# Kernel optimization log

Hardware: AMD Instinct MI355X
Metric: run time of the kernel (lower is better)

## Reference

```python
import jax, jax.numpy as jnp
import numpy as np

N, E, H, HEADS, T = 40000, 320000, 128, 4, 3
DH = H // HEADS


def setup_inputs() -> dict:
    key = jax.random.key(0)
    ks = jax.random.split(key, 32)
    f32 = jnp.float32

    def w(k, shape, s=0.05):
        return (s * jax.random.normal(k, shape)).astype(f32)

    inp = {
        "x": jax.random.normal(ks[0], (N, H), dtype=f32),
        "edge_index": jax.random.randint(ks[1], (2, E), 0, N, dtype=jnp.int32),
        "edge_attr": 0.1 * jax.random.normal(ks[2], (E, H), dtype=f32),
        "wq": w(ks[3], (H, H)), "bq": w(ks[4], (H,)),
        "wk": w(ks[5], (H, H)), "bk": w(ks[6], (H,)),
        "wv": w(ks[7], (H, H)), "bv": w(ks[8], (H,)),
        "w_ao": w(ks[9], (H, H)), "b_ao": w(ks[10], (H,)),
        "ln1_g": jnp.ones((H,), f32), "ln1_b": jnp.zeros((H,), f32),
        "w_int": w(ks[11], (4 * H, H)), "b_int": w(ks[12], (4 * H,)),
        "w_out": w(ks[13], (H, 4 * H)), "b_out": w(ks[14], (H,)),
        "ln2_g": jnp.ones((H,), f32), "ln2_b": jnp.zeros((H,), f32),
        "w_ih": w(ks[15], (3 * H, H)), "w_hh": w(ks[16], (3 * H, H)),
        "b_ih": w(ks[17], (3 * H,)), "b_hh": w(ks[18], (3 * H,)),
        "ln3_g": jnp.ones((H,), f32), "ln3_b": jnp.zeros((H,), f32),
    }
    return inp


def _ln(x, g, b, eps=1e-12):
    u = jnp.mean(x, axis=-1, keepdims=True)
    s = jnp.mean((x - u) ** 2, axis=-1, keepdims=True)
    return g * (x - u) / jnp.sqrt(s + eps) + b


def _gat(x, src, dst, edge_attr, wq, bq, wk, bk, wv, bv):
    # per-edge gather: x_i = target features, x_j = source features (+ pseudo)
    x_i = x[dst]                       # [E, H]
    x_j = x[src] + edge_attr           # [E, H]
    q = (x_i @ wq.T + bq).reshape(-1, HEADS, DH)
    k = (x_j @ wk.T + bk).reshape(-1, HEADS, DH)
    v = (x_j @ wv.T + bv).reshape(-1, HEADS, DH)
    alpha = jnp.sum(q * k, axis=-1) / jnp.sqrt(jnp.float32(DH))  # [E, HEADS]
    # segment softmax over incoming edges of each target node
    m = jax.ops.segment_max(alpha, dst, num_segments=N)
    m = jnp.where(jnp.isfinite(m), m, jnp.zeros_like(m))
    a = jnp.exp(alpha - m[dst])
    s = jax.ops.segment_sum(a, dst, num_segments=N)
    a = a / (s[dst] + 1e-16)
    out = jax.ops.segment_sum(a[..., None] * v, dst, num_segments=N)  # [N, HEADS, DH]
    return out.reshape(N, H)


def reference(x, edge_index, edge_attr, wq, bq, wk, bk, wv, bv,
              w_ao, b_ao, ln1_g, ln1_b, w_int, b_int, w_out, b_out,
              ln2_g, ln2_b, w_ih, w_hh, b_ih, b_hh, ln3_g, ln3_b):
    src, dst = edge_index[0], edge_index[1]
    h = x  # GRU hidden state, [N, H] (seq_len=1, batch=N)
    for _ in range(T):
        att = _gat(x, src, dst, edge_attr, wq, bq, wk, bk, wv, bv)
        att = _ln(att @ w_ao.T + b_ao + x, ln1_g, ln1_b)
        inter = jax.nn.gelu(att @ w_int.T + b_int, approximate=False)
        m = _ln(inter @ w_out.T + b_out + att, ln2_g, ln2_b)
        # single-step GRU (torch gate order: r, z, n)
        gi = m @ w_ih.T + b_ih
        gh = h @ w_hh.T + b_hh
        ir, iz, inn = jnp.split(gi, 3, axis=-1)
        hr, hz, hn = jnp.split(gh, 3, axis=-1)
        r = jax.nn.sigmoid(ir + hr)
        z = jax.nn.sigmoid(iz + hz)
        n = jnp.tanh(inn + r * hn)
        h = (1.0 - z) * n + z * h
        x = _ln(h, ln3_g, ln3_b)
    return x
```

## Files before the change

### kernel.cpp

```cpp
#include <hip/hip_runtime.h>
#include <hip/hip_bf16.h>
#include <math.h>

#define N_NODES 40000
#define N_EDGES 320000
#define T_ITERS 3

typedef __attribute__((ext_vector_type(8))) short short8;
typedef __attribute__((ext_vector_type(4))) short short4v;
typedef __attribute__((ext_vector_type(4))) float f32x4;

static __device__ __forceinline__ short f2bf(float f) {
    union { float f; unsigned u; } x; x.f = f;
    unsigned r = (x.u + 0x7fffu + ((x.u >> 16) & 1u)) >> 16;
    return (short)r;
}
static __device__ __forceinline__ float bf2f(short s) {
    union { unsigned u; float f; } x; x.u = ((unsigned)(unsigned short)s) << 16;
    return x.f;
}

__global__ __launch_bounds__(256) void qkv_kernel(
    const short* __restrict__ A, const short* __restrict__ W,
    const float* __restrict__ bias, short* __restrict__ Cb)
{
    __shared__ __align__(16) short smem[64 * 136];
    short* As = smem;
    short* Ws = smem + 64 * 40;
    short* Cs = smem;

    const int tid  = threadIdx.x;
    const int lane = tid & 63, wid = tid >> 6;
    const int wm = wid & 1, wn = wid >> 1;
    const int t16 = lane & 15, quad = lane >> 4;
    const long blockM = (long)blockIdx.x * 64;
    const int colBase = blockIdx.y * 128;

    f32x4 acc[2][4];
    for (int i = 0; i < 2; i++)
        for (int j = 0; j < 4; j++)
            acc[i][j] = (f32x4){0.f, 0.f, 0.f, 0.f};

    for (int k0 = 0; k0 < 128; k0 += 32) {
        {
            const int r = tid >> 2, c = (tid & 3) * 8;
            *(short8*)&As[r * 40 + c] = *(const short8*)(A + (blockM + r) * 128 + k0 + c);
        }
        for (int gg = 0; gg < 2; gg++) {
            const int chunk = tid + gg * 256;
            const int r = chunk >> 2, c = (chunk & 3) * 8;
            *(short8*)&Ws[r * 40 + c] =
                *(const short8*)(W + (long)(colBase + r) * 128 + k0 + c);
        }
        __syncthreads();
        short8 a0 = *(const short8*)&As[(wm * 32 + t16) * 40 + quad * 8];
        short8 a1 = *(const short8*)&As[(wm * 32 + 16 + t16) * 40 + quad * 8];
        for (int ni = 0; ni < 4; ni++) {
            short8 bf = *(const short8*)&Ws[(wn * 64 + ni * 16 + t16) * 40 + quad * 8];
            acc[0][ni] = __builtin_amdgcn_mfma_f32_16x16x32_bf16(a0, bf, acc[0][ni], 0, 0, 0);
            acc[1][ni] = __builtin_amdgcn_mfma_f32_16x16x32_bf16(a1, bf, acc[1][ni], 0, 0, 0);
        }
        __syncthreads();
    }

    for (int mi = 0; mi < 2; mi++)
        for (int ni = 0; ni < 4; ni++) {
            const int col = wn * 64 + ni * 16 + t16;
            const float bb = bias[colBase + col];
            for (int r = 0; r < 4; r++) {
                const int row = wm * 32 + mi * 16 + quad * 4 + r;
                Cs[row * 136 + col] = f2bf(acc[mi][ni][r] + bb);
            }
        }
    __syncthreads();
    for (int it = 0; it < 4; it++) {
        const int idx = it * 256 + tid;
        const int row = idx >> 4, c8 = idx & 15;
        *(short8*)(Cb + (blockM + row) * 384 + colBase + c8 * 8) =
            *(const short8*)&Cs[row * 136 + c8 * 8];
    }
}

__global__ __launch_bounds__(256, 4) void ekv_kernel(
    const float* __restrict__ ea, const short* __restrict__ Wkv,
    const float* __restrict__ bkv, const int* __restrict__ eids,
    short* __restrict__ EKV)
{
    __shared__ __align__(16) char smem[64 * 136 * 2 + 256 * 40 * 2];
    short* As = (short*)smem;
    short* Ws = (short*)(smem + 64 * 136 * 2);
    short* Cs = (short*)smem;

    const int tid  = threadIdx.x;
    const int lane = tid & 63, wid = tid >> 6;
    const int t16 = lane & 15, quad = lane >> 4;
    const long blockM = (long)blockIdx.x * 64;

    {
        const int r = tid >> 2, c0 = (tid & 3) * 32;
        const long e = eids[blockM + r];
        const float* gp = ea + e * 128 + c0;
        for (int half = 0; half < 2; half++) {
            float4 v0 = *(const float4*)(gp + half * 16);
            float4 v1 = *(const float4*)(gp + half * 16 + 4);
            float4 v2 = *(const float4*)(gp + half * 16 + 8);
            float4 v3 = *(const float4*)(gp + half * 16 + 12);
            short8 s0, s1;
            s0[0] = f2bf(v0.x); s0[1] = f2bf(v0.y); s0[2] = f2bf(v0.z); s0[3] = f2bf(v0.w);
            s0[4] = f2bf(v1.x); s0[5] = f2bf(v1.y); s0[6] = f2bf(v1.z); s0[7] = f2bf(v1.w);
            s1[0] = f2bf(v2.x); s1[1] = f2bf(v2.y); s1[2] = f2bf(v2.z); s1[3] = f2bf(v2.w);
            s1[4] = f2bf(v3.x); s1[5] = f2bf(v3.y); s1[6] = f2bf(v3.z); s1[7] = f2bf(v3.w);
            *(short8*)&As[r * 136 + c0 + half * 16]     = s0;
            *(short8*)&As[r * 136 + c0 + half * 16 + 8] = s1;
        }
    }

    f32x4 acc[4][4];
    for (int i = 0; i < 4; i++)
        for (int j = 0; j < 4; j++)
            acc[i][j] = (f32x4){0.f, 0.f, 0.f, 0.f};

    for (int k0 = 0; k0 < 128; k0 += 32) {
        for (int g = 0; g < 4; g++) {
            const int idx = tid + g * 256;
            const int r = idx >> 2, c = (idx & 3) * 8;
            *(short8*)&Ws[r * 40 + c] = *(const short8*)(Wkv + (long)r * 128 + k0 + c);
        }
        __syncthreads();
        short8 a[4];
        for (int mi = 0; mi < 4; mi++)
            a[mi] = *(const short8*)&As[(mi * 16 + t16) * 136 + k0 + quad * 8];
        for (int ni = 0; ni < 4; ni++) {
            short8 bf = *(const short8*)&Ws[(wid * 64 + ni * 16 + t16) * 40 + quad * 8];
            for (int mi = 0; mi < 4; mi++)
                acc[mi][ni] = __builtin_amdgcn_mfma_f32_16x16x32_bf16(a[mi], bf, acc[mi][ni], 0, 0, 0);
        }
        __syncthreads();
    }

    for (int mi = 0; mi < 4; mi++)
        for (int ni = 0; ni < 4; ni++) {
            const int col = wid * 64 + ni * 16 + t16;
            const float bv_ = bkv[col];
            for (int r = 0; r < 4; r++) {
                const int row = mi * 16 + quad * 4 + r;
                Cs[row * 276 + col] = f2bf(acc[mi][ni][r] + bv_);
            }
        }
    __syncthreads();
    for (int it = 0; it < 8; it++) {
        const int idx = it * 256 + tid;
        const int row = idx >> 5, c8 = idx & 31;
        *(short8*)(EKV + (blockM + row) * 256 + c8 * 8) = *(const short8*)&Cs[row * 276 + c8 * 8];
    }
}

__global__ __launch_bounds__(256) void edge_attn_kernel(
    const short* __restrict__ QKVb, const short* __restrict__ EKV,
    const int* __restrict__ rowptr, const int* __restrict__ esrc,
    short* __restrict__ outb)
{
    const int wid = threadIdx.x >> 6, lane = threadIdx.x & 63;
    const int n = blockIdx.x * 4 + wid;
    if (n >= N_NODES) return;
    const int g = lane >> 3, l8 = lane & 7;
    const int d0 = l8 * 16;
    const float scale = 0.17677669529663687f;

    short8 q0 = *(const short8*)&QKVb[(long)n * 384 + d0];
    short8 q1 = *(const short8*)&QKVb[(long)n * 384 + d0 + 8];
    float qf[16];
#pragma unroll
    for (int j = 0; j < 8; j++) { qf[j] = bf2f(q0[j]); qf[8 + j] = bf2f(q1[j]); }

    const int beg = rowptr[n], end = rowptr[n + 1];
    float acc[16];
#pragma unroll
    for (int j = 0; j < 16; j++) acc[j] = 0.f;
    float ssum = 0.f;

    for (int i0 = beg; i0 < end; i0 += 8) {
        const int i = i0 + g;
        const bool valid = i < end;
        const long ii = valid ? i : beg;
        const long s = esrc[ii];
        short8 k0 = *(const short8*)&EKV[ii * 256 + d0];
        short8 k1 = *(const short8*)&EKV[ii * 256 + d0 + 8];
        short8 xk0 = *(const short8*)&QKVb[s * 384 + 128 + d0];
        short8 xk1 = *(const short8*)&QKVb[s * 384 + 128 + d0 + 8];
        short8 v0 = *(const short8*)&EKV[ii * 256 + 128 + d0];
        short8 v1 = *(const short8*)&EKV[ii * 256 + 128 + d0 + 8];
        short8 xv0 = *(const short8*)&QKVb[s * 384 + 256 + d0];
        short8 xv1 = *(const short8*)&QKVb[s * 384 + 256 + d0 + 8];
        float dot = 0.f;
#pragma unroll
        for (int j = 0; j < 8; j++) {
            dot += qf[j] * (bf2f(k0[j]) + bf2f(xk0[j]));
            dot += qf[8 + j] * (bf2f(k1[j]) + bf2f(xk1[j]));
        }
        dot += __shfl_xor(dot, 1);
        float a = valid ? __expf(dot * scale) : 0.f;
        ssum += a;
#pragma unroll
        for (int j = 0; j < 8; j++) {
            acc[j]     += a * (bf2f(v0[j]) + bf2f(xv0[j]));
            acc[8 + j] += a * (bf2f(v1[j]) + bf2f(xv1[j]));
        }
    }
#pragma unroll
    for (int o = 8; o < 64; o <<= 1) {
#pragma unroll
        for (int j = 0; j < 16; j++) acc[j] += __shfl_xor(acc[j], o);
        ssum += __shfl_xor(ssum, o);
    }
    if (g == 0) {
        float inv = 1.0f / (ssum + 1e-16f);
        short8 o0, o1;
#pragma unroll
        for (int j = 0; j < 8; j++) { o0[j] = f2bf(acc[j] * inv); o1[j] = f2bf(acc[8 + j] * inv); }
        *(short8*)&outb[(long)n * 128 + d0] = o0;
        *(short8*)&outb[(long)n * 128 + d0 + 8] = o1;
    }
}

__global__ __launch_bounds__(256) void ffn_kernel(
    const short* __restrict__ attraw, const short* __restrict__ x,
    const short* __restrict__ Wao, const short* __restrict__ Wint,
    const short* __restrict__ Wout, const float* __restrict__ b_ao,
    const float* __restrict__ b_int, const float* __restrict__ b_out,
    const float* __restrict__ ln1_g, const float* __restrict__ ln1_b,
    const float* __restrict__ ln2_g, const float* __restrict__ ln2_b,
    short* __restrict__ Mout)
{
    __shared__ __align__(16) short As[64 * 136];
    __shared__ __align__(16) short Is[64 * 136];
    __shared__ __align__(16) short Ws[128 * 40];

    const int tid  = threadIdx.x;
    const int lane = tid & 63, wid = tid >> 6;
    const int t16 = lane & 15, quad = lane >> 4;
    const long blockM = (long)blockIdx.x * 64;

    {
        const int r = tid >> 2, c = (tid & 3) * 32;
        const long gr = blockM + r;
        for (int j = 0; j < 4; j++) {
            *(short8*)&As[r * 136 + c + j * 8] = *(const short8*)(x + gr * 128 + c + j * 8);
            *(short8*)&Is[r * 136 + c + j * 8] = *(const short8*)(attraw + gr * 128 + c + j * 8);
        }
    }
    __syncthreads();

    f32x4 acc0[8];
    for (int j = 0; j < 8; j++) acc0[j] = (f32x4){0.f, 0.f, 0.f, 0.f};
    for (int k0 = 0; k0 < 128; k0 += 32) {
        const int r = tid >> 1, c = (tid & 1) * 16;
        *(short8*)&Ws[r * 40 + c]     = *(const short8*)(Wao + (long)r * 128 + k0 + c);
        *(short8*)&Ws[r * 40 + c + 8] = *(const short8*)(Wao + (long)r * 128 + k0 + c + 8);
        __syncthreads();
        short8 a = *(const short8*)&Is[(wid * 16 + t16) * 136 + k0 + quad * 8];
        for (int ni = 0; ni < 8; ni++) {
            short8 bf = *(const short8*)&Ws[(ni * 16 + t16) * 40 + quad * 8];
            acc0[ni] = __builtin_amdgcn_mfma_f32_16x16x32_bf16(a, bf, acc0[ni], 0, 0, 0);
        }
        __syncthreads();
    }
    for (int r = 0; r < 4; r++) {
        const int row = wid * 16 + quad * 4 + r;
        float vals[8];
        float s = 0.f;
        for (int ni = 0; ni < 8; ni++) {
            const int col = ni * 16 + t16;
            float v = acc0[ni][r] + b_ao[col] + bf2f(As[row * 136 + col]);
            vals[ni] = v;
            s += v;
        }
        for (int o = 1; o < 16; o <<= 1) s += __shfl_xor(s, o);
        float u = s * (1.0f / 128.0f);
        float vs = 0.f;
        for (int ni = 0; ni < 8; ni++) { float d = vals[ni] - u; vals[ni] = d; vs += d * d; }
        for (int o = 1; o < 16; o <<= 1) vs += __shfl_xor(vs, o);
        float rstd = rsqrtf(vs * (1.0f / 128.0f) + 1e-12f);
        for (int ni = 0; ni < 8; ni++) {
            const int col = ni * 16 + t16;
            As[row * 136 + col] = f2bf(ln1_g[col] * vals[ni] * rstd + ln1_b[col]);
        }
    }
    __syncthreads();

    f32x4 acc2[8];
    for (int j = 0; j < 8; j++) acc2[j] = (f32x4){0.f, 0.f, 0.f, 0.f};
    for (int kc = 0; kc < 4; kc++) {
        f32x4 acc1[8];
        for (int j = 0; j < 8; j++) acc1[j] = (f32x4){0.f, 0.f, 0.f, 0.f};
        for (int k0 = 0; k0 < 128; k0 += 32) {
            const int r = tid >> 1, c = (tid & 1) * 16;
            *(short8*)&Ws[r * 40 + c] =
                *(const short8*)(Wint + (long)(kc * 128 + r) * 128 + k0 + c);
            *(short8*)&Ws[r * 40 + c + 8] =
                *(const short8*)(Wint + (long)(kc * 128 + r) * 128 + k0 + c + 8);
            __syncthreads();
            short8 a = *(const short8*)&As[(wid * 16 + t16) * 136 + k0 + quad * 8];
            for (int ni = 0; ni < 8; ni++) {
                short8 bf = *(const short8*)&Ws[(ni * 16 + t16) * 40 + quad * 8];
                acc1[ni] = __builtin_amdgcn_mfma_f32_16x16x32_bf16(a, bf, acc1[ni], 0, 0, 0);
            }
            __syncthreads();
        }
        for (int ni = 0; ni < 8; ni++) {
            const int col = ni * 16 + t16;
            const float bi = b_int[kc * 128 + col];
            for (int r = 0; r < 4; r++) {
                const int row = wid * 16 + quad * 4 + r;
                float v = acc1[ni][r] + bi;
                v = 0.5f * v * (1.0f + erff(v * 0.70710678118654752f));
                Is[row * 136 + col] = f2bf(v);
            }
        }
        __syncthreads();
        for (int k0 = 0; k0 < 128; k0 += 32) {
            const int r = tid >> 1, c = (tid & 1) * 16;
            *(short8*)&Ws[r * 40 + c] =
                *(const short8*)(Wout + (long)r * 512 + kc * 128 + k0 + c);
            *(short8*)&Ws[r * 40 + c + 8] =
                *(const short8*)(Wout + (long)r * 512 + kc * 128 + k0 + c + 8);
            __syncthreads();
            short8 a = *(const short8*)&Is[(wid * 16 + t16) * 136 + k0 + quad * 8];
            for (int ni = 0; ni < 8; ni++) {
                short8 bf = *(const short8*)&Ws[(ni * 16 + t16) * 40 + quad * 8];
                acc2[ni] = __builtin_amdgcn_mfma_f32_16x16x32_bf16(a, bf, acc2[ni], 0, 0, 0);
            }
            __syncthreads();
        }
    }

    for (int r = 0; r < 4; r++) {
        const int row = wid * 16 + quad * 4 + r;
        const long gr = blockM + row;
        float vals[8];
        float s = 0.f;
        for (int ni = 0; ni < 8; ni++) {
            const int col = ni * 16 + t16;
            float v = acc2[ni][r] + b_out[col] + bf2f(As[row * 136 + col]);
            vals[ni] = v;
            s += v;
        }
        for (int o = 1; o < 16; o <<= 1) s += __shfl_xor(s, o);
        float u = s * (1.0f / 128.0f);
        float vs = 0.f;
        for (int ni = 0; ni < 8; ni++) { float d = vals[ni] - u; vals[ni] = d; vs += d * d; }
        for (int o = 1; o < 16; o <<= 1) vs += __shfl_xor(vs, o);
        float rstd = rsqrtf(vs * (1.0f / 128.0f) + 1e-12f);
        for (int ni = 0; ni < 8; ni++) {
            const int col = ni * 16 + t16;
            Mout[gr * 128 + col] = f2bf(ln2_g[col] * vals[ni] * rstd + ln2_b[col]);
        }
    }
}

template<bool FINAL>
__global__ __launch_bounds__(256) void gru_kernel(
    const short* __restrict__ m, const short* __restrict__ h,
    const short* __restrict__ Wg, const float* __restrict__ bg,
    const float* __restrict__ g3, const float* __restrict__ b3,
    short* __restrict__ hout, void* __restrict__ xout)
{
    __shared__ __align__(16) char smem[64 * 520 * 2];
    short* As = (short*)smem;
    short* Ws = (short*)(smem + 64 * 40 * 2);
    short* Os = (short*)smem;

    const int tid  = threadIdx.x;
    const int lane = tid & 63, wid = tid >> 6;
    const int t16 = lane & 15, quad = lane >> 4;
    const long blockM = (long)blockIdx.x * 64;

    f32x4 acc[4][8];
    for (int i = 0; i < 4; i++)
        for (int j = 0; j < 8; j++)
            acc[i][j] = (f32x4){0.f, 0.f, 0.f, 0.f};

    for (int k0 = 0; k0 < 256; k0 += 32) {
        const short* src = (k0 < 128) ? m : h;
        {
            const int r = tid >> 2, c = (tid & 3) * 8;
            *(short8*)&As[r * 40 + c] =
                *(const short8*)(src + (blockM + r) * 128 + (k0 & 127) + c);
        }
        for (int g = 0; g < 8; g++) {
            const int idx = tid + g * 256;
            const int r = idx >> 2, c = (idx & 3) * 8;
            *(short8*)&Ws[r * 40 + c] = *(const short8*)(Wg + (long)r * 256 + k0 + c);
        }
        __syncthreads();
        short8 a[4];
        for (int mi = 0; mi < 4; mi++)
            a[mi] = *(const short8*)&As[(mi * 16 + t16) * 40 + quad * 8];
        for (int ni = 0; ni < 8; ni++) {
            short8 bf = *(const short8*)&Ws[(wid * 128 + ni * 16 + t16) * 40 + quad * 8];
            for (int mi = 0; mi < 4; mi++)
                acc[mi][ni] = __builtin_amdgcn_mfma_f32_16x16x32_bf16(a[mi], bf, acc[mi][ni], 0, 0, 0);
        }
        __syncthreads();
    }

    for (int mi = 0; mi < 4; mi++)
        for (int ni = 0; ni < 8; ni++) {
            const int col = wid * 128 + ni * 16 + t16;
            const float bb = bg[col];
            for (int r = 0; r < 4; r++) {
                const int row = mi * 16 + quad * 4 + r;
                Os[row * 520 + col] = f2bf(acc[mi][ni][r] + bb);
            }
        }
    __syncthreads();

    {
        const int row = tid >> 2;
        const int c0 = (tid & 3) * 32;
        const long gr = blockM + row;
        float hv[32];
        for (int j = 0; j < 4; j++) {
            short8 hpv = *(const short8*)(h + gr * 128 + c0 + j * 8);
            short8 orv = *(const short8*)&Os[row * 520 + c0 + j * 8];
            short8 ozv = *(const short8*)&Os[row * 520 + 128 + c0 + j * 8];
            short8 onv = *(const short8*)&Os[row * 520 + 256 + c0 + j * 8];
            short8 ohv = *(const short8*)&Os[row * 520 + 384 + c0 + j * 8];
            for (int q = 0; q < 8; q++) {
                float rr = 1.f / (1.f + __expf(-bf2f(orv[q])));
                float zz = 1.f / (1.f + __expf(-bf2f(ozv[q])));
                float nn = tanhf(bf2f(onv[q]) + rr * bf2f(ohv[q]));
                float hpq = bf2f(hpv[q]);
                hv[j * 8 + q] = (1.f - zz) * nn + zz * hpq;
            }
        }
        float s = 0.f;
        for (int j = 0; j < 32; j++) s += hv[j];
        s += __shfl_xor(s, 1); s += __shfl_xor(s, 2);
        float u = s * (1.0f / 128.0f);
        float vs = 0.f;
        for (int j = 0; j < 32; j++) { float d = hv[j] - u; vs += d * d; }
        vs += __shfl_xor(vs, 1); vs += __shfl_xor(vs, 2);
        float rstd = rsqrtf(vs * (1.0f / 128.0f) + 1e-12f);
        for (int j = 0; j < 4; j++) {
            short8 o;
            for (int q = 0; q < 8; q++) o[q] = f2bf(hv[j * 8 + q]);
            *(short8*)(hout + gr * 128 + c0 + j * 8) = o;
        }
        if (FINAL) {
            float* xo = (float*)xout;
            for (int j = 0; j < 8; j++) {
                float4 o;
                o.x = g3[c0 + j * 4 + 0] * (hv[j * 4 + 0] - u) * rstd + b3[c0 + j * 4 + 0];
                o.y = g3[c0 + j * 4 + 1] * (hv[j * 4 + 1] - u) * rstd + b3[c0 + j * 4 + 1];
                o.z = g3[c0 + j * 4 + 2] * (hv[j * 4 + 2] - u) * rstd + b3[c0 + j * 4 + 2];
                o.w = g3[c0 + j * 4 + 3] * (hv[j * 4 + 3] - u) * rstd + b3[c0 + j * 4 + 3];
                *(float4*)&xo[gr * 128 + c0 + j * 4] = o;
            }
        } else {
            short* xo = (short*)xout;
            for (int j = 0; j < 4; j++) {
                short8 o;
                for (int q = 0; q < 8; q++) {
                    const int c = c0 + j * 8 + q;
                    o[q] = f2bf(g3[c] * (hv[j * 8 + q] - u) * rstd + b3[c]);
                }
                *(short8*)(xo + gr * 128 + c0 + j * 8) = o;
            }
        }
    }
}

__global__ void count_kernel(const int* __restrict__ dst, int* __restrict__ cnt) {
    int e = blockIdx.x * 256 + threadIdx.x;
    if (e < N_EDGES) atomicAdd(&cnt[dst[e]], 1);
}

__global__ __launch_bounds__(1024) void scan_kernel(const int* __restrict__ cnt,
                                                    int* __restrict__ rowptr) {
    __shared__ int lds[1024];
    const int tid = threadIdx.x;
    const int CH = 40;
    const int base = tid * CH;
    int sum = 0;
    for (int j = 0; j < CH; j++) { int i = base + j; if (i < N_NODES) sum += cnt[i]; }
    lds[tid] = sum;
    __syncthreads();
    for (int off = 1; off < 1024; off <<= 1) {
        int v = (tid >= off) ? lds[tid - off] : 0;
        __syncthreads();
        lds[tid] += v;
        __syncthreads();
    }
    int run = lds[tid] - sum;
    for (int j = 0; j < CH; j++) {
        int i = base + j;
        if (i < N_NODES) { rowptr[i] = run; run += cnt[i]; }
    }
    if (tid == 1023) rowptr[N_NODES] = lds[1023];
}

__global__ void fill_kernel(const int* __restrict__ src, const int* __restrict__ dst,
                            const int* __restrict__ rowptr, int* __restrict__ wo,
                            int* __restrict__ esrc, int* __restrict__ eids) {
    int e = blockIdx.x * 256 + threadIdx.x;
    if (e < N_EDGES) {
        int d = dst[e];
        int pos = atomicAdd(&wo[d], 1);
        int slot = rowptr[d] + pos;
        esrc[slot] = src[e];
        eids[slot] = e;
    }
}

__global__ void sortfix_kernel(const int* __restrict__ rowptr,
                               int* __restrict__ eids, int* __restrict__ esrc) {
    int n = blockIdx.x * 256 + threadIdx.x;
    if (n >= N_NODES) return;
    const int beg = rowptr[n], end = rowptr[n + 1];
    for (int i = beg + 1; i < end; i++) {
        int ke = eids[i], ks = esrc[i];
        int j = i - 1;
        while (j >= beg && eids[j] > ke) {
            eids[j + 1] = eids[j];
            esrc[j + 1] = esrc[j];
            j--;
        }
        eids[j + 1] = ke;
        esrc[j + 1] = ks;
    }
}

__global__ void cvt_kernel(const float* __restrict__ s, short* __restrict__ d, int n) {
    int i = (blockIdx.x * 256 + threadIdx.x) * 4;
    if (i < n) {
        float4 v = *(const float4*)(s + i);
        short4v sv;
        sv.x = f2bf(v.x); sv.y = f2bf(v.y); sv.z = f2bf(v.z); sv.w = f2bf(v.w);
        *(short4v*)(d + i) = sv;
    }
}
__global__ void bias_cat_kernel(const float* __restrict__ bq, const float* __restrict__ bk,
                                const float* __restrict__ bv, float* __restrict__ bqkv,
                                float* __restrict__ bkv) {
    int i = blockIdx.x * 256 + threadIdx.x;
    if (i < 384) bqkv[i] = (i < 128) ? bq[i] : 0.0f;
    if (i < 256) bkv[i] = (i < 128) ? bk[i] : bv[i - 128];
}
__global__ void build_wg_kernel(const float* __restrict__ wih, const float* __restrict__ whh,
                                const float* __restrict__ bih, const float* __restrict__ bhh,
                                short* __restrict__ Wg, float* __restrict__ bg) {
    int idx = blockIdx.x * 256 + threadIdx.x;
    if (idx < 512 * 256) {
        int r = idx >> 8, k = idx & 255;
        float v;
        if (r < 256)      v = (k < 128) ? wih[r * 128 + k] : whh[r * 128 + k - 128];
        else if (r < 384) v = (k < 128) ? wih[r * 128 + k] : 0.f;
        else              v = (k < 128) ? 0.f : whh[(r - 128) * 128 + k - 128];
        Wg[idx] = f2bf(v);
    }
    if (idx < 512) {
        float b;
        if (idx < 256)      b = bih[idx] + bhh[idx];
        else if (idx < 384) b = bih[idx];
        else                b = bhh[idx - 128];
        bg[idx] = b;
    }
}

extern "C" void kernel_launch(void* const* d_in, const int* in_sizes, int n_in,
                              void* d_out, int out_size, void* d_ws, size_t ws_size,
                              hipStream_t stream) {
    const float* x_in  = (const float*)d_in[0];
    const int*   eidx  = (const int*)d_in[1];
    const float* ea    = (const float*)d_in[2];
    const float* wq    = (const float*)d_in[3];
    const float* bq    = (const float*)d_in[4];
    const float* wk    = (const float*)d_in[5];
    const float* bk    = (const float*)d_in[6];
    const float* wv    = (const float*)d_in[7];
    const float* bv    = (const float*)d_in[8];
    const float* w_ao  = (const float*)d_in[9];
    const float* b_ao  = (const float*)d_in[10];
    const float* ln1_g = (const float*)d_in[11];
    const float* ln1_b = (const float*)d_in[12];
    const float* w_int = (const float*)d_in[13];
    const float* b_int = (const float*)d_in[14];
    const float* w_out = (const float*)d_in[15];
    const float* b_out = (const float*)d_in[16];
    const float* ln2_g = (const float*)d_in[17];
    const float* ln2_b = (const float*)d_in[18];
    const float* w_ih  = (const float*)d_in[19];
    const float* w_hh  = (const float*)d_in[20];
    const float* b_ih  = (const float*)d_in[21];
    const float* b_hh  = (const float*)d_in[22];
    const float* ln3_g = (const float*)d_in[23];
    const float* ln3_b = (const float*)d_in[24];
    const int* srcv = eidx;
    const int* dstv = eidx + N_EDGES;

    char* ws = (char*)d_ws;
    size_t off = 0;
    auto alloc = [&](size_t bytes) -> void* {
        void* p = ws + off;
        off += (bytes + 255) & ~(size_t)255;
        return p;
    };
    short* EKV  = (short*)alloc((size_t)N_EDGES * 256 * 2);
    short* Wcat = (short*)alloc(384 * 128 * 2);
    short* Wao  = (short*)alloc(128 * 128 * 2);
    short* Wint = (short*)alloc(512 * 128 * 2);
    short* Wout = (short*)alloc(128 * 512 * 2);
    short* Wg   = (short*)alloc(512 * 256 * 2);
    float* bqkv = (float*)alloc(384 * 4);
    float* bkv  = (float*)alloc(256 * 4);
    float* bg   = (float*)alloc(512 * 4);
    int* cnt    = (int*)alloc((size_t)N_NODES * 4);
    int* wo     = (int*)alloc((size_t)N_NODES * 4);
    int* rowptr = (int*)alloc((size_t)(N_NODES + 1) * 4);
    int* esrc   = (int*)alloc((size_t)N_EDGES * 4);
    int* eids   = (int*)alloc((size_t)N_EDGES * 4);
    short* xb     = (short*)alloc((size_t)N_NODES * 128 * 2);
    short* QKVb   = (short*)alloc((size_t)N_NODES * 384 * 2);
    short* attraw = (short*)alloc((size_t)N_NODES * 128 * 2);
    short* mbuf   = (short*)alloc((size_t)N_NODES * 128 * 2);
    short* hbuf   = (short*)alloc((size_t)N_NODES * 128 * 2);
    short* xbuf   = (short*)alloc((size_t)N_NODES * 128 * 2);
    if (off > ws_size) return;

    cvt_kernel<<<16, 256, 0, stream>>>(wq, Wcat, 16384);
    cvt_kernel<<<16, 256, 0, stream>>>(wk, Wcat + 16384, 16384);
    cvt_kernel<<<16, 256, 0, stream>>>(wv, Wcat + 32768, 16384);
    cvt_kernel<<<16, 256, 0, stream>>>(w_ao, Wao, 16384);
    cvt_kernel<<<64, 256, 0, stream>>>(w_int, Wint, 65536);
    cvt_kernel<<<64, 256, 0, stream>>>(w_out, Wout, 65536);
    cvt_kernel<<<5000, 256, 0, stream>>>(x_in, xb, N_NODES * 128);
    bias_cat_kernel<<<2, 256, 0, stream>>>(bq, bk, bv, bqkv, bkv);
    build_wg_kernel<<<512, 256, 0, stream>>>(w_ih, w_hh, b_ih, b_hh, Wg, bg);

    hipMemsetAsync(cnt, 0, (size_t)N_NODES * 4, stream);
    hipMemsetAsync(wo, 0, (size_t)N_NODES * 4, stream);
    count_kernel<<<1250, 256, 0, stream>>>(dstv, cnt);
    scan_kernel<<<1, 1024, 0, stream>>>(cnt, rowptr);
    fill_kernel<<<1250, 256, 0, stream>>>(srcv, dstv, rowptr, wo, esrc, eids);
    sortfix_kernel<<<157, 256, 0, stream>>>(rowptr, eids, esrc);

    ekv_kernel<<<5000, 256, 0, stream>>>(ea, Wcat + 128 * 128, bkv, eids, EKV);

    const short* xcur = xb;
    const short* hcur = xb;
    for (int t = 0; t < T_ITERS; t++) {
        qkv_kernel<<<dim3(625, 3), 256, 0, stream>>>(xcur, Wcat, bqkv, QKVb);
        edge_attn_kernel<<<10000, 256, 0, stream>>>(QKVb, EKV, rowptr, esrc, attraw);
        ffn_kernel<<<625, 256, 0, stream>>>(
            attraw, xcur, Wao, Wint, Wout, b_ao, b_int, b_out,
            ln1_g, ln1_b, ln2_g, ln2_b, mbuf);
        if (t == T_ITERS - 1)
            gru_kernel<true><<<625, 256, 0, stream>>>(
                mbuf, hcur, Wg, bg, ln3_g, ln3_b, hbuf, d_out);
        else
            gru_kernel<false><<<625, 256, 0, stream>>>(
                mbuf, hcur, Wg, bg, ln3_g, ln3_b, hbuf, xbuf);
        xcur = xbuf;
        hcur = hbuf;
    }
}
```

Before: 1.191 ms.

## Keep hidden state and x in fp32 and restructure GRU kernel without LDS

Hidden state and the normalized x now stay in fp32 instead of bf16, with the qkv and GRU kernels converting to bf16 on load. The qkv kernel stages the whole 64x128 A tile in shared memory once rather than per k-chunk. The GRU kernel is rewritten so each wave keeps its A fragments in registers and reads weights straight from global memory, with the gates and layernorm computed in registers without the LDS round trip. The goal appears to be accuracy plus lower LDS and sync overhead, at the cost of twice the bytes for x and h traffic and uncached per-wave weight reads.

```diff
diff --git a/kernel.cpp b/kernel.cpp
--- a/kernel.cpp
+++ b/kernel.cpp
@@ -21,12 +21,12 @@
 }
 
 __global__ __launch_bounds__(256) void qkv_kernel(
-    const short* __restrict__ A, const short* __restrict__ W,
+    const float* __restrict__ A, const short* __restrict__ W,
     const float* __restrict__ bias, short* __restrict__ Cb)
 {
-    __shared__ __align__(16) short smem[64 * 136];
+    __shared__ __align__(16) short smem[64 * 136 + 128 * 40];
     short* As = smem;
-    short* Ws = smem + 64 * 40;
+    short* Ws = smem + 64 * 136;
     short* Cs = smem;
 
     const int tid  = threadIdx.x;
@@ -36,16 +36,30 @@
     const long blockM = (long)blockIdx.x * 64;
     const int colBase = blockIdx.y * 128;
 
+    {
+        const int r = tid >> 2, c0 = (tid & 3) * 32;
+        const float* gp = A + (blockM + r) * 128 + c0;
+        for (int half = 0; half < 2; half++) {
+            float4 v0 = *(const float4*)(gp + half * 16);
+            float4 v1 = *(const float4*)(gp + half * 16 + 4);
+            float4 v2 = *(const float4*)(gp + half * 16 + 8);
+            float4 v3 = *(const float4*)(gp + half * 16 + 12);
+            short8 s0, s1;
+            s0[0] = f2bf(v0.x); s0[1] = f2bf(v0.y); s0[2] = f2bf(v0.z); s0[3] = f2bf(v0.w);
+            s0[4] = f2bf(v1.x); s0[5] = f2bf(v1.y); s0[6] = f2bf(v1.z); s0[7] = f2bf(v1.w);
+            s1[0] = f2bf(v2.x); s1[1] = f2bf(v2.y); s1[2] = f2bf(v2.z); s1[3] = f2bf(v2.w);
+            s1[4] = f2bf(v3.x); s1[5] = f2bf(v3.y); s1[6] = f2bf(v3.z); s1[7] = f2bf(v3.w);
+            *(short8*)&As[r * 136 + c0 + half * 16]     = s0;
+            *(short8*)&As[r * 136 + c0 + half * 16 + 8] = s1;
+        }
+    }
+
     f32x4 acc[2][4];
     for (int i = 0; i < 2; i++)
         for (int j = 0; j < 4; j++)
             acc[i][j] = (f32x4){0.f, 0.f, 0.f, 0.f};
 
     for (int k0 = 0; k0 < 128; k0 += 32) {
-        {
-            const int r = tid >> 2, c = (tid & 3) * 8;
-            *(short8*)&As[r * 40 + c] = *(const short8*)(A + (blockM + r) * 128 + k0 + c);
-        }
         for (int gg = 0; gg < 2; gg++) {
             const int chunk = tid + gg * 256;
             const int r = chunk >> 2, c = (chunk & 3) * 8;
@@ -53,8 +67,8 @@
                 *(const short8*)(W + (long)(colBase + r) * 128 + k0 + c);
         }
         __syncthreads();
-        short8 a0 = *(const short8*)&As[(wm * 32 + t16) * 40 + quad * 8];
-        short8 a1 = *(const short8*)&As[(wm * 32 + 16 + t16) * 40 + quad * 8];
+        short8 a0 = *(const short8*)&As[(wm * 32 + t16) * 136 + k0 + quad * 8];
+        short8 a1 = *(const short8*)&As[(wm * 32 + 16 + t16) * 136 + k0 + quad * 8];
         for (int ni = 0; ni < 4; ni++) {
             short8 bf = *(const short8*)&Ws[(wn * 64 + ni * 16 + t16) * 40 + quad * 8];
             acc[0][ni] = __builtin_amdgcn_mfma_f32_16x16x32_bf16(a0, bf, acc[0][ni], 0, 0, 0);
@@ -224,7 +238,7 @@
 }
 
 __global__ __launch_bounds__(256) void ffn_kernel(
-    const short* __restrict__ attraw, const short* __restrict__ x,
+    const short* __restrict__ attraw, const float* __restrict__ x,
     const short* __restrict__ Wao, const short* __restrict__ Wint,
     const short* __restrict__ Wout, const float* __restrict__ b_ao,
     const float* __restrict__ b_int, const float* __restrict__ b_out,
@@ -244,10 +258,8 @@
     {
         const int r = tid >> 2, c = (tid & 3) * 32;
         const long gr = blockM + r;
-        for (int j = 0; j < 4; j++) {
-            *(short8*)&As[r * 136 + c + j * 8] = *(const short8*)(x + gr * 128 + c + j * 8);
+        for (int j = 0; j < 4; j++)
             *(short8*)&Is[r * 136 + c + j * 8] = *(const short8*)(attraw + gr * 128 + c + j * 8);
-        }
     }
     __syncthreads();
 
@@ -265,13 +277,15 @@
         }
         __syncthreads();
     }
+    float attv[4][8];
     for (int r = 0; r < 4; r++) {
         const int row = wid * 16 + quad * 4 + r;
+        const long gr = blockM + row;
         float vals[8];
         float s = 0.f;
         for (int ni = 0; ni < 8; ni++) {
             const int col = ni * 16 + t16;
-            float v = acc0[ni][r] + b_ao[col] + bf2f(As[row * 136 + col]);
+            float v = acc0[ni][r] + b_ao[col] + x[gr * 128 + col];
             vals[ni] = v;
             s += v;
         }
@@ -283,7 +297,9 @@
         float rstd = rsqrtf(vs * (1.0f / 128.0f) + 1e-12f);
         for (int ni = 0; ni < 8; ni++) {
             const int col = ni * 16 + t16;
-            As[row * 136 + col] = f2bf(ln1_g[col] * vals[ni] * rstd + ln1_b[col]);
+            float av = ln1_g[col] * vals[ni] * rstd + ln1_b[col];
+            attv[r][ni] = av;
+            As[row * 136 + col] = f2bf(av);
         }
     }
     __syncthreads();
@@ -341,7 +357,7 @@
         float s = 0.f;
         for (int ni = 0; ni < 8; ni++) {
             const int col = ni * 16 + t16;
-            float v = acc2[ni][r] + b_out[col] + bf2f(As[row * 136 + col]);
+            float v = acc2[ni][r] + b_out[col] + attv[r][ni];
             vals[ni] = v;
             s += v;
         }
@@ -358,115 +374,106 @@
     }
 }
 
-template<bool FINAL>
-__global__ __launch_bounds__(256) void gru_kernel(
-    const short* __restrict__ m, const short* __restrict__ h,
+__global__ __launch_bounds__(256, 2) void gru_kernel(
+    const short* __restrict__ m, const float* __restrict__ h,
     const short* __restrict__ Wg, const float* __restrict__ bg,
     const float* __restrict__ g3, const float* __restrict__ b3,
-    short* __restrict__ hout, void* __restrict__ xout)
+    float* __restrict__ hout, float* __restrict__ xout)
 {
-    __shared__ __align__(16) char smem[64 * 520 * 2];
-    short* As = (short*)smem;
-    short* Ws = (short*)(smem + 64 * 40 * 2);
-    short* Os = (short*)smem;
-
     const int tid  = threadIdx.x;
     const int lane = tid & 63, wid = tid >> 6;
     const int t16 = lane & 15, quad = lane >> 4;
     const long blockM = (long)blockIdx.x * 64;
+    const long rowA = blockM + wid * 16 + t16;
+
+    short8 a[8];
+#pragma unroll
+    for (int k0 = 0; k0 < 4; k0++)
+        a[k0] = *(const short8*)(m + rowA * 128 + k0 * 32 + quad * 8);
+#pragma unroll
+    for (int k0 = 4; k0 < 8; k0++) {
+        const float* hp8 = h + rowA * 128 + (k0 - 4) * 32 + quad * 8;
+        float4 f0 = *(const float4*)(hp8);
+        float4 f1 = *(const float4*)(hp8 + 4);
+        short8 s;
+        s[0] = f2bf(f0.x); s[1] = f2bf(f0.y); s[2] = f2bf(f0.z); s[3] = f2bf(f0.w);
+        s[4] = f2bf(f1.x); s[5] = f2bf(f1.y); s[6] = f2bf(f1.z); s[7] = f2bf(f1.w);
+        a[k0] = s;
+    }
 
     f32x4 acc[4][8];
-    for (int i = 0; i < 4; i++)
-        for (int j = 0; j < 8; j++)
-            acc[i][j] = (f32x4){0.f, 0.f, 0.f, 0.f};
-
-    for (int k0 = 0; k0 < 256; k0 += 32) {
-        const short* src = (k0 < 128) ? m : h;
-        {
-            const int r = tid >> 2, c = (tid & 3) * 8;
-            *(short8*)&As[r * 40 + c] =
-                *(const short8*)(src + (blockM + r) * 128 + (k0 & 127) + c);
-        }
-        for (int g = 0; g < 8; g++) {
-            const int idx = tid + g * 256;
-            const int r = idx >> 2, c = (idx & 3) * 8;
-            *(short8*)&Ws[r * 40 + c] = *(const short8*)(Wg + (long)r * 256 + k0 + c);
-        }
-        __syncthreads();
-        short8 a[4];
-        for (int mi = 0; mi < 4; mi++)
-            a[mi] = *(const short8*)&As[(mi * 16 + t16) * 40 + quad * 8];
-        for (int ni = 0; ni < 8; ni++) {
-            short8 bf = *(const short8*)&Ws[(wid * 128 + ni * 16 + t16) * 40 + quad * 8];
-            for (int mi = 0; mi < 4; mi++)
-                acc[mi][ni] = __builtin_amdgcn_mfma_f32_16x16x32_bf16(a[mi], bf, acc[mi][ni], 0, 0, 0);
-        }
-        __syncthreads();
-    }
-
-    for (int mi = 0; mi < 4; mi++)
-        for (int ni = 0; ni < 8; ni++) {
-            const int col = wid * 128 + ni * 16 + t16;
-            const float bb = bg[col];
-            for (int r = 0; r < 4; r++) {
-                const int row = mi * 16 + quad * 4 + r;
-                Os[row * 520 + col] = f2bf(acc[mi][ni][r] + bb);
+#pragma unroll
+    for (int g = 0; g < 4; g++)
+#pragma unroll
+        for (int c16 = 0; c16 < 8; c16++)
+            acc[g][c16] = (f32x4){0.f, 0.f, 0.f, 0.f};
+
+#pragma unroll
+    for (int g = 0; g < 4; g++)
+#pragma unroll
+        for (int c16 = 0; c16 < 8; c16++) {
+            const short* wr = Wg + (long)(g * 128 + c16 * 16 + t16) * 256 + quad * 8;
+#pragma unroll
+            for (int k0 = 0; k0 < 8; k0++) {
+                short8 w = *(const short8*)(wr + k0 * 32);
+                acc[g][c16] = __builtin_amdgcn_mfma_f32_16x16x32_bf16(a[k0], w, acc[g][c16], 0, 0, 0);
             }
         }
-    __syncthreads();
-
-    {
-        const int row = tid >> 2;
-        const int c0 = (tid & 3) * 32;
-        const long gr = blockM + row;
-        float hv[32];
-        for (int j = 0; j < 4; j++) {
-            short8 hpv = *(const short8*)(h + gr * 128 + c0 + j * 8);
-            short8 orv = *(const short8*)&Os[row * 520 + c0 + j * 8];
-            short8 ozv = *(const short8*)&Os[row * 520 + 128 + c0 + j * 8];
-            short8 onv = *(const short8*)&Os[row * 520 + 256 + c0 + j * 8];
-            short8 ohv = *(const short8*)&Os[row * 520 + 384 + c0 + j * 8];
-            for (int q = 0; q < 8; q++) {
-                float rr = 1.f / (1.f + __expf(-bf2f(orv[q])));
-                float zz = 1.f / (1.f + __expf(-bf2f(ozv[q])));
-                float nn = tanhf(bf2f(onv[q]) + rr * bf2f(ohv[q]));
-                float hpq = bf2f(hpv[q]);
-                hv[j * 8 + q] = (1.f - zz) * nn + zz * hpq;
-            }
-        }
-        float s = 0.f;
-        for (int j = 0; j < 32; j++) s += hv[j];
-        s += __shfl_xor(s, 1); s += __shfl_xor(s, 2);
-        float u = s * (1.0f / 128.0f);
-        float vs = 0.f;
-        for (int j = 0; j < 32; j++) { float d = hv[j] - u; vs += d * d; }
-        vs += __shfl_xor(vs, 1); vs += __shfl_xor(vs, 2);
-        float rstd = rsqrtf(vs * (1.0f / 128.0f) + 1e-12f);
-        for (int j = 0; j < 4; j++) {
-            short8 o;
-            for (int q = 0; q < 8; q++) o[q] = f2bf(hv[j * 8 + q]);
-            *(short8*)(hout + gr * 128 + c0 + j * 8) = o;
-        }
-        if (FINAL) {
-            float* xo = (float*)xout;
-            for (int j = 0; j < 8; j++) {
-                float4 o;
-                o.x = g3[c0 + j * 4 + 0] * (hv[j * 4 + 0] - u) * rstd + b3[c0 + j * 4 + 0];
-                o.y = g3[c0 + j * 4 + 1] * (hv[j * 4 + 1] - u) * rstd + b3[c0 + j * 4 + 1];
-                o.z = g3[c0 + j * 4 + 2] * (hv[j * 4 + 2] - u) * rstd + b3[c0 + j * 4 + 2];
-                o.w = g3[c0 + j * 4 + 3] * (hv[j * 4 + 3] - u) * rstd + b3[c0 + j * 4 + 3];
-                *(float4*)&xo[gr * 128 + c0 + j * 4] = o;
-            }
-        } else {
-            short* xo = (short*)xout;
-            for (int j = 0; j < 4; j++) {
-                short8 o;
-                for (int q = 0; q < 8; q++) {
-                    const int c = c0 + j * 8 + q;
-                    o[q] = f2bf(g3[c] * (hv[j * 8 + q] - u) * rstd + b3[c]);
-                }
-                *(short8*)(xo + gr * 128 + c0 + j * 8) = o;
-            }
+
+    const long rowBase = blockM + wid * 16 + quad * 4;
+    float hv[8][4];
+    float sums[4] = {0.f, 0.f, 0.f, 0.f};
+#pragma unroll
+    for (int c16 = 0; c16 < 8; c16++) {
+        const int col = c16 * 16 + t16;
+        const float b_r = bg[col];
+        const float b_z = bg[col + 128];
+        const float b_i = bg[col + 256];
+        const float b_h = bg[col + 384];
+#pragma unroll
+        for (int r = 0; r < 4; r++) {
+            float rr = 1.f / (1.f + __expf(-(acc[0][c16][r] + b_r)));
+            float zz = 1.f / (1.f + __expf(-(acc[1][c16][r] + b_z)));
+            float nn = tanhf(acc[2][c16][r] + b_i + rr * (acc[3][c16][r] + b_h));
+            float hp = h[(rowBase + r) * 128 + col];
+            float v = (1.f - zz) * nn + zz * hp;
+            hv[c16][r] = v;
+            sums[r] += v;
+        }
+    }
+#pragma unroll
+    for (int r = 0; r < 4; r++)
+#pragma unroll
+        for (int o = 1; o < 16; o <<= 1) sums[r] += __shfl_xor(sums[r], o);
+    float u[4], vsum[4] = {0.f, 0.f, 0.f, 0.f};
+#pragma unroll
+    for (int r = 0; r < 4; r++) u[r] = sums[r] * (1.0f / 128.0f);
+#pragma unroll
+    for (int c16 = 0; c16 < 8; c16++)
+#pragma unroll
+        for (int r = 0; r < 4; r++) {
+            float d = hv[c16][r] - u[r];
+            vsum[r] += d * d;
+        }
+#pragma unroll
+    for (int r = 0; r < 4; r++) {
+#pragma unroll
+        for (int o = 1; o < 16; o <<= 1) vsum[r] += __shfl_xor(vsum[r], o);
+    }
+    float rstd[4];
+#pragma unroll
+    for (int r = 0; r < 4; r++)
+        rstd[r] = rsqrtf(vsum[r] * (1.0f / 128.0f) + 1e-12f);
+
+#pragma unroll
+    for (int c16 = 0; c16 < 8; c16++) {
+        const int col = c16 * 16 + t16;
+        const float gg = g3[col], bb = b3[col];
+#pragma unroll
+        for (int r = 0; r < 4; r++) {
+            const long gr = rowBase + r;
+            hout[gr * 128 + col] = hv[c16][r];
+            xout[gr * 128 + col] = gg * (hv[c16][r] - u[r]) * rstd[r] + bb;
         }
     }
 }
@@ -620,12 +627,12 @@
     int* rowptr = (int*)alloc((size_t)(N_NODES + 1) * 4);
     int* esrc   = (int*)alloc((size_t)N_EDGES * 4);
     int* eids   = (int*)alloc((size_t)N_EDGES * 4);
-    short* xb     = (short*)alloc((size_t)N_NODES * 128 * 2);
     short* QKVb   = (short*)alloc((size_t)N_NODES * 384 * 2);
     short* attraw = (short*)alloc((size_t)N_NODES * 128 * 2);
     short* mbuf   = (short*)alloc((size_t)N_NODES * 128 * 2);
-    short* hbuf   = (short*)alloc((size_t)N_NODES * 128 * 2);
-    short* xbuf   = (short*)alloc((size_t)N_NODES * 128 * 2);
+    float* xbuf   = (float*)alloc((size_t)N_NODES * 128 * 4);
+    float* ha     = (float*)alloc((size_t)N_NODES * 128 * 4);
+    float* hb     = (float*)alloc((size_t)N_NODES * 128 * 4);
     if (off > ws_size) return;
 
     cvt_kernel<<<16, 256, 0, stream>>>(wq, Wcat, 16384);
@@ -634,7 +641,6 @@
     cvt_kernel<<<16, 256, 0, stream>>>(w_ao, Wao, 16384);
     cvt_kernel<<<64, 256, 0, stream>>>(w_int, Wint, 65536);
     cvt_kernel<<<64, 256, 0, stream>>>(w_out, Wout, 65536);
-    cvt_kernel<<<5000, 256, 0, stream>>>(x_in, xb, N_NODES * 128);
     bias_cat_kernel<<<2, 256, 0, stream>>>(bq, bk, bv, bqkv, bkv);
     build_wg_kernel<<<512, 256, 0, stream>>>(w_ih, w_hh, b_ih, b_hh, Wg, bg);
 
@@ -647,21 +653,19 @@
 
     ekv_kernel<<<5000, 256, 0, stream>>>(ea, Wcat + 128 * 128, bkv, eids, EKV);
 
-    const short* xcur = xb;
-    const short* hcur = xb;
+    const float* xcur = x_in;
+    const float* hcur = x_in;
+    float* hping[2] = {ha, hb};
     for (int t = 0; t < T_ITERS; t++) {
         qkv_kernel<<<dim3(625, 3), 256, 0, stream>>>(xcur, Wcat, bqkv, QKVb);
         edge_attn_kernel<<<10000, 256, 0, stream>>>(QKVb, EKV, rowptr, esrc, attraw);
         ffn_kernel<<<625, 256, 0, stream>>>(
             attraw, xcur, Wao, Wint, Wout, b_ao, b_int, b_out,
             ln1_g, ln1_b, ln2_g, ln2_b, mbuf);
-        if (t == T_ITERS - 1)
-            gru_kernel<true><<<625, 256, 0, stream>>>(
-                mbuf, hcur, Wg, bg, ln3_g, ln3_b, hbuf, d_out);
-        else
-            gru_kernel<false><<<625, 256, 0, stream>>>(
-                mbuf, hcur, Wg, bg, ln3_g, ln3_b, hbuf, xbuf);
+        float* xo = (t == T_ITERS - 1) ? (float*)d_out : xbuf;
+        gru_kernel<<<625, 256, 0, stream>>>(
+            mbuf, hcur, Wg, bg, ln3_g, ln3_b, hping[t & 1], xo);
+        hcur = hping[t & 1];
         xcur = xbuf;
-        hcur = hbuf;
-    }
-}
+    }
+}
```

Result: slower. 1.239 ms (+4.0%).
